# Kernel tuning notes

Hardware: AMD Instinct MI355X
Metric: run time of the kernel (lower is better)

The kernel has to match this reference:

```python
import jax, jax.numpy as jnp
import numpy as np

L, BS, H, W, C, NH = 6, 2, 48, 192, 128, 8
DIM = C // NH
EPS_LN = 1e-5
EPS_LA = 1e-6


def layer_norm(x, g, b):
    m = x.mean(-1, keepdims=True)
    v = ((x - m) ** 2).mean(-1, keepdims=True)
    return (x - m) / jnp.sqrt(v + EPS_LN) * g + b


def lin(x, w):
    # torch nn.Linear convention: y = x @ W^T
    return jnp.einsum('...i,oi->...o', x, w)


def linear_attention(q, k, v):
    # LoFTR-style kernelized attention: phi(x) = elu(x) + 1
    Q = jax.nn.elu(q) + 1.0
    K = jax.nn.elu(k) + 1.0
    KV = jnp.einsum('nshd,nshv->nhdv', K, v)            # [n, nh, d, d]
    Z = 1.0 / (jnp.einsum('nlhd,nhd->nlh', Q, K.sum(1)) + EPS_LA)
    return jnp.einsum('nlhd,nhdv,nlh->nlhv', Q, KV, Z)  # [n, l, nh, d]


def full_attention(q, k, v):
    scale = 1.0 / np.sqrt(q.shape[-1])
    qk = jnp.einsum('nlhd,nshd->nlsh', q, k) * scale    # [n, l, s, nh]
    A = jax.nn.softmax(qk, axis=2)
    out = jnp.einsum('nlsh,nshd->nlhd', A, v)
    return out, A


def self_layer(x, p):
    bs, h, w, c = x.shape
    xf = x.reshape(bs, h * w, c)
    xn = layer_norm(xf, p['n1_g'], p['n1_b'])
    q = lin(xn, p['q']).reshape(bs, h * w, NH, DIM)
    k = lin(xn, p['k']).reshape(bs, h * w, NH, DIM)
    v = lin(xn, p['v']).reshape(bs, h * w, NH, DIM)
    msg = linear_attention(q, k, v).reshape(bs, h * w, c)
    msg = xf + lin(msg, p['merge'])
    mn = layer_norm(msg, p['n2_g'], p['n2_b'])
    mn = lin(jax.nn.gelu(lin(mn, p['mlp1']), approximate=False), p['mlp2'])
    return (msg + mn).reshape(bs, h, w, c)


def cross_layer(fl, fr, p):
    bs, h, w, c = fl.shape
    fln = layer_norm(fl, p['n1_g'], p['n1_b'])
    frn = layer_norm(fr, p['n1_g'], p['n1_b'])

    def proj(x, wm):
        return lin(x, wm).reshape(bs * h, w, NH, DIM)

    ql, kl, vl = proj(fln, p['q']), proj(fln, p['k']), proj(fln, p['v'])
    qr, kr, vr = proj(frn, p['q']), proj(frn, p['k']), proj(frn, p['v'])

    def half(feat, q, k, v):
        msg, A = full_attention(q, k, v)
        raw = A.sum(-1).reshape(bs, h, w, w)
        m = feat + lin(msg.reshape(bs, h, w, c), p['merge'])
        mn = layer_norm(m, p['n2_g'], p['n2_b'])
        mn = lin(jax.nn.gelu(lin(mn, p['mlp1']), approximate=False), p['mlp2'])
        return m + mn, raw

    ml, raw_l = half(fl, ql, kr, vr)
    mr, raw_r = half(fr, qr, kl, vl)
    return ml, mr, raw_l, raw_r


PARAM_NAMES = ['q', 'k', 'v', 'merge', 'mlp1', 'mlp2']
VEC_NAMES = ['n1_g', 'n1_b', 'n2_g', 'n2_b']


def setup_inputs() -> dict:
    key = jax.random.key(0)
    ks = jax.random.split(key, 16)
    s = 1.0 / np.sqrt(C)
    inp = {
        'feat_left': jax.random.normal(ks[0], (BS, H, W, C), jnp.float32),
        'feat_right': jax.random.normal(ks[1], (BS, H, W, C), jnp.float32),
        'attn_left': jnp.zeros((BS, H, W, W), jnp.float32),
        'attn_right': jnp.zeros((BS, H, W, W), jnp.float32),
    }
    for i, nm in enumerate(PARAM_NAMES):
        inp['sa_' + nm] = jax.random.normal(ks[2 + i], (L, C, C), jnp.float32) * s
        inp['ca_' + nm] = jax.random.normal(ks[8 + i], (L, C, C), jnp.float32) * s
    for nm in VEC_NAMES:
        fill = jnp.ones if nm.endswith('_g') else jnp.zeros
        inp['sa_' + nm] = fill((L, C), jnp.float32)
        inp['ca_' + nm] = fill((L, C), jnp.float32)
    return inp


def reference(feat_left, feat_right, attn_left, attn_right,
              sa_q, sa_k, sa_v, sa_merge, sa_mlp1, sa_mlp2,
              sa_n1_g, sa_n1_b, sa_n2_g, sa_n2_b,
              ca_q, ca_k, ca_v, ca_merge, ca_mlp1, ca_mlp2,
              ca_n1_g, ca_n1_b, ca_n2_g, ca_n2_b):
    sa = {'q': sa_q, 'k': sa_k, 'v': sa_v, 'merge': sa_merge, 'mlp1': sa_mlp1,
          'mlp2': sa_mlp2, 'n1_g': sa_n1_g, 'n1_b': sa_n1_b, 'n2_g': sa_n2_g, 'n2_b': sa_n2_b}
    ca = {'q': ca_q, 'k': ca_k, 'v': ca_v, 'merge': ca_merge, 'mlp1': ca_mlp1,
          'mlp2': ca_mlp2, 'n1_g': ca_n1_g, 'n1_b': ca_n1_b, 'n2_g': ca_n2_g, 'n2_b': ca_n2_b}
    fl, fr, al, ar = feat_left, feat_right, attn_left, attn_right
    for i in range(L):
        p_sa = {k_: v_[i] for k_, v_ in sa.items()}
        p_ca = {k_: v_[i] for k_, v_ in ca.items()}
        fl = self_layer(fl, p_sa)
        fr = self_layer(fr, p_sa)
        fl, fr, raw_l, raw_r = cross_layer(fl, fr, p_ca)
        al = al + raw_l
        ar = ar + raw_r
    return fl, fr, (al, ar)
```

## Files before the change

kernel.cpp:

```cpp
#include <hip/hip_runtime.h>
#include <hip/hip_bf16.h>

using bf16x8 = __attribute__((ext_vector_type(8))) short;
using bf16x4 = __attribute__((ext_vector_type(4))) short;
using f32x4  = __attribute__((ext_vector_type(4))) float;

#define NE      4718592
#define HALF_R  18432
#define HALF_E  2359296
#define ATTN_E  3538944
#define SEQ     9216
#define NCHUNK  18
#define VSTRIDE 3088
#define RB_G    3136

typedef const unsigned int __attribute__((address_space(1)))* gas_u32;
typedef unsigned int __attribute__((address_space(3)))* las_u32;

__device__ __forceinline__ float b2f(short s) {
  union { unsigned u; float f; } x; x.u = ((unsigned)(unsigned short)s) << 16; return x.f;
}
__device__ __forceinline__ short f2b(float f) {
  __hip_bfloat16 h = __float2bfloat16(f);
  short s; __builtin_memcpy(&s, &h, 2); return s;
}
__device__ __forceinline__ f32x4 mfma16(bf16x8 a, bf16x8 b, f32x4 c) {
  return __builtin_amdgcn_mfma_f32_16x16x32_bf16(a, b, c, 0, 0, 0);
}
__device__ __forceinline__ f32x4 mfma16k16(bf16x4 a, bf16x4 b, f32x4 c) {
#if __has_builtin(__builtin_amdgcn_mfma_f32_16x16x16bf16_1k)
  return __builtin_amdgcn_mfma_f32_16x16x16bf16_1k(a, b, c, 0, 0, 0);
#else
  f32x4 d;
  asm("v_mfma_f32_16x16x16_bf16 %0, %1, %2, %3" : "=v"(d) : "v"(a), "v"(b), "v"(c));
  return d;
#endif
}

#define TR_READ12(V0,V1,V2,V3,V4,V5,V6,V7,V8,V9,V10,V11, ADDR) \
  asm volatile( \
    "ds_read_b64_tr_b16 %0, %12 offset:0\n\t" \
    "ds_read_b64_tr_b16 %1, %12 offset:512\n\t" \
    "ds_read_b64_tr_b16 %2, %12 offset:1024\n\t" \
    "ds_read_b64_tr_b16 %3, %12 offset:1536\n\t" \
    "ds_read_b64_tr_b16 %4, %12 offset:2048\n\t" \
    "ds_read_b64_tr_b16 %5, %12 offset:2560\n\t" \
    "ds_read_b64_tr_b16 %6, %12 offset:3072\n\t" \
    "ds_read_b64_tr_b16 %7, %12 offset:3584\n\t" \
    "ds_read_b64_tr_b16 %8, %12 offset:4096\n\t" \
    "ds_read_b64_tr_b16 %9, %12 offset:4608\n\t" \
    "ds_read_b64_tr_b16 %10, %12 offset:5120\n\t" \
    "ds_read_b64_tr_b16 %11, %12 offset:5632\n\t" \
    "s_waitcnt lgkmcnt(0)" \
    : "=&v"(V0), "=&v"(V1), "=&v"(V2), "=&v"(V3), "=&v"(V4), "=&v"(V5), \
      "=&v"(V6), "=&v"(V7), "=&v"(V8), "=&v"(V9), "=&v"(V10), "=&v"(V11) \
    : "v"(ADDR))

__global__ void k_w2b(const float* s0, const float* s1, const float* s2, const float* s3,
                      const float* s4, const float* s5, const float* s6, const float* s7,
                      const float* s8, const float* s9, const float* s10, const float* s11,
                      short* __restrict__ dst) {
  const float* srcs[12] = {s0,s1,s2,s3,s4,s5,s6,s7,s8,s9,s10,s11};
  const float* src = srcs[blockIdx.y];
  short* d = dst + (size_t)blockIdx.y*6*16384;
  int idx = blockIdx.x*256 + threadIdx.x;
  int layer = idx >> 11, w = idx & 2047;
  int c = w >> 4, gp = w & 15;
  int gs = gp ^ (c & 7);
  const float* s = src + layer*16384 + c*128 + gs*8;
  f32x4 v0 = *(const f32x4*)(s);
  f32x4 v1 = *(const f32x4*)(s + 4);
  short tmp[8];
  tmp[0]=f2b(v0[0]); tmp[1]=f2b(v0[1]); tmp[2]=f2b(v0[2]); tmp[3]=f2b(v0[3]);
  tmp[4]=f2b(v1[0]); tmp[5]=f2b(v1[1]); tmp[6]=f2b(v1[2]); tmp[7]=f2b(v1[3]);
  bf16x8 pk; __builtin_memcpy(&pk, tmp, 16);
  *(bf16x8*)(d + layer*16384 + c*128 + gp*8) = pk;
}

__device__ __forceinline__ void stage_W_async(const short* __restrict__ Wt, short* Ws,
                                              int wave, int lane) {
  #pragma unroll
  for (int is = 0; is < 8; is++) {
    int chunk = is*4 + wave;
    __builtin_amdgcn_global_load_lds((gas_u32)(const void*)(Wt + chunk*512 + lane*8),
                                     (las_u32)(void*)(Ws + chunk*512), 16, 0, 0);
  }
}
__device__ __forceinline__ void mfma_core_regA(const bf16x8 af[4], const short* Ws,
                                               int lane, f32x4 acc[8]) {
  int lrow = lane & 15, lgrp = lane >> 4;
  #pragma unroll
  for (int ct = 0; ct < 8; ct++) {
    int c = ct*16 + lrow;
    #pragma unroll
    for (int kc = 0; kc < 4; kc++) {
      int g = (kc*4 + lgrp) ^ (c & 7);
      bf16x8 wf = *(const bf16x8*)(&Ws[c*128 + g*8]);
      acc[ct] = mfma16(wf, af[kc], acc[ct]);
    }
  }
}
__device__ __forceinline__ void mfma_core_T(const short* As, const short* Ws,
                                            int wave, int lane, f32x4 acc[8]) {
  int lrow = lane & 15, lgrp = lane >> 4;
  bf16x8 af[4];
  int rl = wave*16 + lrow;
  #pragma unroll
  for (int kc = 0; kc < 4; kc++) {
    int g = (kc*4 + lgrp) ^ (rl & 7);
    af[kc] = *(const bf16x8*)(&As[rl*128 + g*8]);
  }
  mfma_core_regA(af, Ws, lane, acc);
}

__global__ __launch_bounds__(256) void k_qkv3(const float* __restrict__ FL,
                                              const float* __restrict__ FR,
                                              const short* __restrict__ Wq,
                                              const short* __restrict__ Wk,
                                              const short* __restrict__ Wv,
                                              const float* __restrict__ g,
                                              const float* __restrict__ b,
                                              short* __restrict__ Qo,
                                              short* __restrict__ Ko,
                                              short* __restrict__ Vo,
                                              int phi_mask, float qscale) {
  __shared__ short Ws[128*128];
  int tid = threadIdx.x;
  int row0 = blockIdx.x * 64;
  int wave = tid >> 6, lane = tid & 63;
  int lrow = lane & 15, lgrp = lane >> 4;
  int rl = wave*16 + lrow;
  int row = row0 + rl;
  const float* Fb = (row0 < HALF_R) ? FL : (FR - (size_t)HALF_E);
  stage_W_async(Wq, Ws, wave, lane);
  float x[4][8];
  const float* fr = Fb + (size_t)row*128;
  #pragma unroll
  for (int kc = 0; kc < 4; kc++) {
    f32x4 v0 = *(const f32x4*)(fr + kc*32 + lgrp*8);
    f32x4 v1 = *(const f32x4*)(fr + kc*32 + lgrp*8 + 4);
    x[kc][0]=v0[0]; x[kc][1]=v0[1]; x[kc][2]=v0[2]; x[kc][3]=v0[3];
    x[kc][4]=v1[0]; x[kc][5]=v1[1]; x[kc][6]=v1[2]; x[kc][7]=v1[3];
  }
  float s = 0.f, sq = 0.f;
  #pragma unroll
  for (int kc = 0; kc < 4; kc++)
    #pragma unroll
    for (int j = 0; j < 8; j++) { float xx = x[kc][j]; s += xx; sq += xx*xx; }
  s += __shfl_xor(s, 16, 64); sq += __shfl_xor(sq, 16, 64);
  s += __shfl_xor(s, 32, 64); sq += __shfl_xor(sq, 32, 64);
  float mean = s * (1.f/128.f);
  float var  = sq * (1.f/128.f) - mean*mean;
  float inv  = rsqrtf(var + 1e-5f);
  bf16x8 af[4];
  #pragma unroll
  for (int kc = 0; kc < 4; kc++) {
    int c0 = kc*32 + lgrp*8;
    f32x4 g0 = *(const f32x4*)(g + c0), g1 = *(const f32x4*)(g + c0 + 4);
    f32x4 b0 = *(const f32x4*)(b + c0), b1 = *(const f32x4*)(b + c0 + 4);
    short t8[8];
    t8[0]=f2b((x[kc][0]-mean)*inv*g0[0]+b0[0]); t8[1]=f2b((x[kc][1]-mean)*inv*g0[1]+b0[1]);
    t8[2]=f2b((x[kc][2]-mean)*inv*g0[2]+b0[2]); t8[3]=f2b((x[kc][3]-mean)*inv*g0[3]+b0[3]);
    t8[4]=f2b((x[kc][4]-mean)*inv*g1[0]+b1[0]); t8[5]=f2b((x[kc][5]-mean)*inv*g1[1]+b1[1]);
    t8[6]=f2b((x[kc][6]-mean)*inv*g1[2]+b1[2]); t8[7]=f2b((x[kc][7]-mean)*inv*g1[3]+b1[3]);
    __builtin_memcpy(&af[kc], t8, 16);
  }
  const short* Wp[3] = {Wq, Wk, Wv};
  short* Op[3] = {Qo, Ko, Vo};
  for (int y = 0; y < 3; y++) {
    __syncthreads();
    f32x4 acc[8] = {};
    mfma_core_regA(af, Ws, lane, acc);
    bool phi = (phi_mask >> y) & 1;
    float sc = (y == 0) ? qscale : 1.0f;
    short* OUT = Op[y] + (size_t)row*128 + lgrp*4;
    __syncthreads();
    if (y < 2) stage_W_async(Wp[y+1], Ws, wave, lane);
    #pragma unroll
    for (int ct = 0; ct < 8; ct++) {
      short t4[4];
      #pragma unroll
      for (int reg = 0; reg < 4; reg++) {
        float v = acc[ct][reg] * sc;
        if (phi) v = (v > 0.f) ? v + 1.0f : __expf(v);
        t4[reg] = f2b(v);
      }
      bf16x4 pk; __builtin_memcpy(&pk, t4, 8);
      *(bf16x4*)(OUT + ct*16) = pk;
    }
  }
}

template<bool REGA>
__device__ __forceinline__ void mlp_tail(const bf16x8 af1[4], short* As, short* Ws,
                                         const short* __restrict__ W1,
                                         const short* __restrict__ W2,
                                         const float* __restrict__ g,
                                         const float* __restrict__ b,
                                         const float* __restrict__ Fin,
                                         float* __restrict__ Fout,
                                         int row0, int tid) {
  int wave = tid >> 6, lane = tid & 63;
  int lrow = lane & 15, lgrp = lane >> 4;
  int rl = wave*16 + lrow;
  int orow = row0 + rl;
  const float* Fri = Fin + (size_t)orow*128 + lgrp*4;
  float* Fro = Fout + (size_t)orow*128 + lgrp*4;
  f32x4 acc[8] = {};
  if (REGA) mfma_core_regA(af1, Ws, lane, acc);
  else      mfma_core_T(As, Ws, wave, lane, acc);
  f32x4 fnew[8];
  #pragma unroll
  for (int ct = 0; ct < 8; ct++) {
    f32x4 fv = *(const f32x4*)(Fri + ct*16);
    fnew[ct] = acc[ct] + fv;
  }
  float s = 0.f, sq = 0.f;
  #pragma unroll
  for (int ct = 0; ct < 8; ct++)
    #pragma unroll
    for (int reg = 0; reg < 4; reg++) { float x = fnew[ct][reg]; s += x; sq += x*x; }
  s += __shfl_xor(s, 16, 64); sq += __shfl_xor(sq, 16, 64);
  s += __shfl_xor(s, 32, 64); sq += __shfl_xor(sq, 32, 64);
  float mean = s * (1.f/128.f);
  float var  = sq * (1.f/128.f) - mean*mean;
  float inv  = rsqrtf(var + 1e-5f);
  __syncthreads();
  stage_W_async(W1, Ws, wave, lane);
  #pragma unroll
  for (int ct = 0; ct < 8; ct++) {
    short t4[4];
    #pragma unroll
    for (int reg = 0; reg < 4; reg++) {
      int c = ct*16 + lgrp*4 + reg;
      t4[reg] = f2b((fnew[ct][reg] - mean) * inv * g[c] + b[c]);
    }
    bf16x4 pk; __builtin_memcpy(&pk, t4, 8);
    int G = ct*2 + (lgrp >> 1);
    *(bf16x4*)(&As[rl*128 + ((G ^ (rl & 7))*8) + (lgrp & 1)*4]) = pk;
  }
  __syncthreads();
  f32x4 acc2[8] = {};
  mfma_core_T(As, Ws, wave, lane, acc2);
  __syncthreads();
  stage_W_async(W2, Ws, wave, lane);
  #pragma unroll
  for (int ct = 0; ct < 8; ct++) {
    short t4[4];
    #pragma unroll
    for (int reg = 0; reg < 4; reg++) {
      float v = acc2[ct][reg];
      v = 0.5f*v*(1.0f + erff(v*0.70710678118654752f));
      t4[reg] = f2b(v);
    }
    bf16x4 pk; __builtin_memcpy(&pk, t4, 8);
    int G = ct*2 + (lgrp >> 1);
    *(bf16x4*)(&As[rl*128 + ((G ^ (rl & 7))*8) + (lgrp & 1)*4]) = pk;
  }
  __syncthreads();
  f32x4 acc3[8] = {};
  mfma_core_T(As, Ws, wave, lane, acc3);
  #pragma unroll
  for (int ct = 0; ct < 8; ct++) {
    f32x4 o = fnew[ct] + acc3[ct];
    *(f32x4*)(Fro + ct*16) = o;
  }
}

__global__ __launch_bounds__(256) void k_mlp(const short* __restrict__ Msg,
                                             const short* __restrict__ Wm,
                                             const short* __restrict__ W1,
                                             const short* __restrict__ W2,
                                             const float* __restrict__ g,
                                             const float* __restrict__ b,
                                             const float* __restrict__ Fin,
                                             float* __restrict__ Fout) {
  __shared__ short As[64*128];
  __shared__ short Ws[128*128];
  int tid = threadIdx.x;
  int row0 = blockIdx.x * 64;
  int wave = tid >> 6, lane = tid & 63;
  int lgrp = lane >> 4;
  int row = row0 + wave*16 + (lane & 15);
  stage_W_async(Wm, Ws, wave, lane);
  bf16x8 af1[4];
  const short* mr = Msg + (size_t)row*128;
  #pragma unroll
  for (int kc = 0; kc < 4; kc++)
    af1[kc] = *(const bf16x8*)(mr + kc*32 + lgrp*8);
  __syncthreads();
  mlp_tail<true>(af1, As, Ws, W1, W2, g, b, Fin, Fout, row0, tid);
}

__global__ __launch_bounds__(256) void k_mlp_self(const short* __restrict__ Q,
                                                  const float* __restrict__ kvp,
                                                  const short* __restrict__ Wm,
                                                  const short* __restrict__ W1,
                                                  const short* __restrict__ W2,
                                                  const float* __restrict__ g,
                                                  const float* __restrict__ b,
                                                  const float* __restrict__ FL,
                                                  const float* __restrict__ FR,
                                                  float* __restrict__ Fout) {
  __shared__ short As[64*128];
  __shared__ short Ws[128*128];
  __shared__ float kvs[8*273];
  int tid = threadIdx.x;
  int row0 = blockIdx.x * 64;
  int n = row0 / SEQ;
  const float* Fin = (row0 < HALF_R) ? FL : (FR - (size_t)HALF_E);
  stage_W_async(Wm, Ws, tid >> 6, tid & 63);
  for (int i = tid; i < 8*272; i += 256) {
    int h = i / 272, j = i % 272;
    const float* src = kvp + ((size_t)(n*8 + h)*NCHUNK)*272 + j;
    float s = 0.f;
    #pragma unroll
    for (int c2 = 0; c2 < NCHUNK; c2++) s += src[(size_t)c2*272];
    kvs[h*273 + j] = s;
  }
  __syncthreads();
  int r = tid >> 2, qq = tid & 3;
  const short* qr = Q + (size_t)(row0 + r)*128;
  #pragma unroll
  for (int hh = 0; hh < 2; hh++) {
    int h = qq*2 + hh;
    bf16x8 q0 = *(const bf16x8*)(qr + h*16);
    bf16x8 q1 = *(const bf16x8*)(qr + h*16 + 8);
    float q[16];
    #pragma unroll
    for (int j = 0; j < 8; j++) { q[j] = b2f(q0[j]); q[8+j] = b2f(q1[j]); }
    const float* kvh = kvs + h*273;
    float z = 1e-6f;
    #pragma unroll
    for (int d = 0; d < 16; d++) z += q[d] * kvh[256 + d];
    float invz = 1.f / z;
    short o16[16];
    #pragma unroll
    for (int d2 = 0; d2 < 16; d2++) {
      float o = 0.f;
      #pragma unroll
      for (int d = 0; d < 16; d++) o += q[d] * kvh[d*16 + d2];
      o16[d2] = f2b(o * invz);
    }
    bf16x8 lo, hi; __builtin_memcpy(&lo, o16, 16); __builtin_memcpy(&hi, o16+8, 16);
    *(bf16x8*)(&As[r*128 + (((2*h)   ^ (r & 7))*8)]) = lo;
    *(bf16x8*)(&As[r*128 + (((2*h+1) ^ (r & 7))*8)]) = hi;
  }
  __syncthreads();
  mlp_tail<false>(nullptr, As, Ws, W1, W2, g, b, Fin, Fout, row0, tid);
}

__global__ __launch_bounds__(256) void k_linred(const short* __restrict__ K,
                                                const short* __restrict__ V,
                                                float* __restrict__ kvp) {
  int nh = blockIdx.x;
  int n = nh >> 3, h = nh & 7;
  int chunk = blockIdx.y;
  int r0 = chunk * (SEQ / NCHUNK);
  __shared__ float ks[64][17], vs[64][17];
  int tid = threadIdx.x;
  int d1 = tid >> 4, d2 = tid & 15;
  int rr = tid >> 2, q = tid & 3;
  float kv = 0.f, ksum = 0.f;
  for (int r = r0; r < r0 + SEQ/NCHUNK; r += 64) {
    __syncthreads();
    bf16x4 kk = *(const bf16x4*)(K + (size_t)(n*SEQ + r + rr)*128 + h*16 + q*4);
    bf16x4 vv = *(const bf16x4*)(V + (size_t)(n*SEQ + r + rr)*128 + h*16 + q*4);
    #pragma unroll
    for (int j = 0; j < 4; j++) { ks[rr][q*4+j] = b2f(kk[j]); vs[rr][q*4+j] = b2f(vv[j]); }
    __syncthreads();
    #pragma unroll
    for (int j = 0; j < 64; j++) {
      float kvl = ks[j][d1];
      kv   += kvl * vs[j][d2];
      ksum += kvl;
    }
  }
  float* dst = kvp + ((size_t)nh*NCHUNK + chunk)*272;
  dst[d1*16 + d2] = kv;
  if (d2 == 0) dst[256 + d1] = ksum;
}

__global__ __launch_bounds__(512, 4) void k_fullattn(const short* __restrict__ Q,
                                                     const short* __restrict__ K,
                                                     const short* __restrict__ V,
                                                     short* __restrict__ MSG,
                                                     const float* __restrict__ RSL,
                                                     const float* __restrict__ RSR,
                                                     float* __restrict__ RDL,
                                                     float* __restrict__ RDR,
                                                     const float* __restrict__ ATL,
                                                     const float* __restrict__ ATR,
                                                     int first, int last) {
  __shared__ __attribute__((aligned(16))) char smem[4*RB_G*4];
  short* Vsub = (short*)smem;
  float* rawb = (float*)smem;
  int flat = blockIdx.x;
  int xcd = flat & 7, slot = flat >> 3;
  int group = xcd*24 + (slot >> 2);
  int part = slot & 3;
  int side = group >= 96 ? 1 : 0;
  int n = group - side*96;
  int qbase = side*HALF_R + n*192;
  int kbase = (side^1)*HALF_R + n*192;
  const float* rsb = (side ? RSR : RSL) + (size_t)n*192*192;
  float* rdb = (side ? RDR : RDL) + (size_t)n*192*192;
  const float* atb = (side ? ATR : ATL) + (size_t)n*192*192;
  int tid = threadIdx.x;
  int wave = tid >> 6, lane = tid & 63;
  int lrow = lane & 15, lgrp = lane >> 4;

  #pragma unroll
  for (int i = 0; i < 6; i++) {
    int c = tid + 512*i;
    int s = c >> 4, t8 = c & 15;
    bf16x8 v8 = *(const bf16x8*)(V + (size_t)(kbase + s)*128 + t8*8);
    *(bf16x8*)(&Vsub[(t8 >> 1)*VSTRIDE + s*16 + (t8 & 1)*8]) = v8;
  }
  __syncthreads();

  bf16x4 vf[12];
  {
    unsigned va = (unsigned)(uintptr_t)(&Vsub[0]) + wave*(VSTRIDE*2) + lane*8;
    TR_READ12(vf[0], vf[1], vf[2], vf[3], vf[4], vf[5],
              vf[6], vf[7], vf[8], vf[9], vf[10], vf[11], va);
  }
  __builtin_amdgcn_sched_barrier(0);
  bf16x4 kfr[12];
  #pragma unroll
  for (int st = 0; st < 12; st++)
    kfr[st] = *(const bf16x4*)(K + (size_t)(kbase + st*16 + lrow)*128
                                 + wave*16 + lgrp*4);
  __syncthreads();

  const f32x4 z4 = {0.f, 0.f, 0.f, 0.f};
  int g = wave & 3;
  for (int li = 0; li < 3; li++) {
    int l0 = (part*3 + li)*16;
    bf16x4 qf = *(const bf16x4*)(Q + (size_t)(qbase + l0 + lrow)*128 + wave*16 + lgrp*4);
    f32x4 sa[12];
    #pragma unroll
    for (int st = 0; st < 12; st++)
      sa[st] = mfma16k16(kfr[st], qf, z4);
    float m = -1e30f;
    #pragma unroll
    for (int st = 0; st < 12; st++)
      m = fmaxf(m, fmaxf(fmaxf(sa[st][0], sa[st][1]), fmaxf(sa[st][2], sa[st][3])));
    m = fmaxf(m, __shfl_xor(m, 16, 64));
    m = fmaxf(m, __shfl_xor(m, 32, 64));
    float sum = 0.f;
    #pragma unroll
    for (int st = 0; st < 12; st++) {
      #pragma unroll
      for (int r = 0; r < 4; r++) {
        float p = __expf(sa[st][r] - m);
        sa[st][r] = p; sum += p;
      }
    }
    sum += __shfl_xor(sum, 16, 64);
    sum += __shfl_xor(sum, 32, 64);
    float inv = 1.f / sum;
    #pragma unroll
    for (int st = 0; st < 12; st++) {
      sa[st][0] *= inv; sa[st][1] *= inv; sa[st][2] *= inv; sa[st][3] *= inv;
    }
    {
      f32x4 o = z4;
      #pragma unroll
      for (int st = 0; st < 12; st++) {
        bf16x4 pf;
        pf[0] = f2b(sa[st][0]); pf[1] = f2b(sa[st][1]);
        pf[2] = f2b(sa[st][2]); pf[3] = f2b(sa[st][3]);
        o = mfma16k16(vf[st], pf, o);
      }
      bf16x4 o4;
      o4[0] = f2b(o[0]); o4[1] = f2b(o[1]); o4[2] = f2b(o[2]); o4[3] = f2b(o[3]);
      *(bf16x4*)(MSG + (size_t)(qbase + l0 + lrow)*128 + wave*16 + lgrp*4) = o4;
    }
    if (wave < 4) {
      #pragma unroll
      for (int st = 0; st < 12; st++)
        *(f32x4*)(&rawb[g*RB_G + (lrow*49 + st*4 + lgrp)*4]) = sa[st];
    }
    __syncthreads();
    if (wave >= 4) {
      #pragma unroll
      for (int st = 0; st < 12; st++) {
        f32x4* slot2 = (f32x4*)(&rawb[g*RB_G + (lrow*49 + st*4 + lgrp)*4]);
        *slot2 = *slot2 + sa[st];
      }
    }
    __syncthreads();
    #pragma unroll
    for (int i = 0; i < 2; i++) {
      int sl = tid + 512*i;
      if (sl < 768) {
        int row = sl / 48, grp = sl - row*48;
        int off = (row*49 + grp)*4;
        f32x4 a = *(const f32x4*)(&rawb[0*RB_G + off]);
        f32x4 b = *(const f32x4*)(&rawb[1*RB_G + off]);
        f32x4 c = *(const f32x4*)(&rawb[2*RB_G + off]);
        f32x4 d = *(const f32x4*)(&rawb[3*RB_G + off]);
        f32x4 t = (a + b) + (c + d);
        size_t goff = (size_t)(l0 + row)*192 + grp*4;
        if (!first) t = t + *(const f32x4*)(rsb + goff);
        if (last)   t = t + *(const f32x4*)(atb + goff);
        *(f32x4*)(rdb + goff) = t;
      }
    }
    __syncthreads();
  }
}

extern "C" void kernel_launch(void* const* d_in, const int* in_sizes, int n_in,
                              void* d_out, int out_size, void* d_ws, size_t ws_size,
                              hipStream_t stream) {
  const float* feat_l = (const float*)d_in[0];
  const float* feat_r = (const float*)d_in[1];
  const float* attn_l = (const float*)d_in[2];
  const float* attn_r = (const float*)d_in[3];
  const float* saw[6] = { (const float*)d_in[4],  (const float*)d_in[6],  (const float*)d_in[8],
                          (const float*)d_in[10], (const float*)d_in[12], (const float*)d_in[14] };
  const float* caw[6] = { (const float*)d_in[5],  (const float*)d_in[7],  (const float*)d_in[9],
                          (const float*)d_in[11], (const float*)d_in[13], (const float*)d_in[15] };
  const float* sa_n1g = (const float*)d_in[16]; const float* ca_n1g = (const float*)d_in[17];
  const float* sa_n1b = (const float*)d_in[18]; const float* ca_n1b = (const float*)d_in[19];
  const float* sa_n2g = (const float*)d_in[20]; const float* ca_n2g = (const float*)d_in[21];
  const float* sa_n2b = (const float*)d_in[22]; const float* ca_n2b = (const float*)d_in[23];

  float* F   = (float*)d_ws;
  float* ALa = F + NE;
  float* ARa = ALa + ATTN_E;
  float* KVp = ARa + ATTN_E;
  short* WB  = (short*)(KVp + 32*NCHUNK*272);
  short* Qb  = WB + 12*6*16384;
  short* Kb  = Qb + NE;
  short* Vb  = Kb + NE;
  short* Mb  = Vb + NE;

  float* out = (float*)d_out;

  k_w2b<<<dim3(48,12), 256, 0, stream>>>(saw[0],saw[1],saw[2],saw[3],saw[4],saw[5],
                                         caw[0],caw[1],caw[2],caw[3],caw[4],caw[5], WB);

  for (int i = 0; i < 6; i++) {
    const short* sw[6], *cw[6];
    for (int t = 0; t < 6; t++) { sw[t] = WB + (size_t)(t*6 + i)*16384; cw[t] = WB + (size_t)((6+t)*6 + i)*16384; }
    int vo = i*128;
    const float* FL = (i == 0) ? feat_l : F;
    const float* FR = (i == 0) ? feat_r : (F + HALF_E);
    k_qkv3<<<576, 256, 0, stream>>>(FL, FR, sw[0], sw[1], sw[2], sa_n1g+vo, sa_n1b+vo,
                                    Qb, Kb, Vb, 0b011, 1.0f);
    k_linred<<<dim3(32, NCHUNK), 256, 0, stream>>>(Kb, Vb, KVp);
    k_mlp_self<<<576, 256, 0, stream>>>(Qb, KVp, sw[3], sw[4], sw[5],
                                        sa_n2g+vo, sa_n2b+vo, FL, FR, F);
    k_qkv3<<<576, 256, 0, stream>>>(F, F + HALF_E, cw[0], cw[1], cw[2],
                                    ca_n1g+vo, ca_n1b+vo, Qb, Kb, Vb, 0, 0.25f);
    int last = (i == 5);
    k_fullattn<<<768, 512, 0, stream>>>(Qb, Kb, Vb, Mb,
                                        ALa, ARa,
                                        last ? out + NE : ALa,
                                        last ? out + NE + ATTN_E : ARa,
                                        attn_l, attn_r,
                                        i == 0 ? 1 : 0, last);
    k_mlp<<<576, 256, 0, stream>>>(Mb, cw[3], cw[4], cw[5], ca_n2g+vo, ca_n2b+vo,
                                   F, last ? out : F);
  }
}
```

Baseline: 976.8 us.

## Fuse next-stage LayerNorm and QKV projection into MLP tail kernels

The separate QKV projection kernels run after each MLP are removed. The MLP tail kernels now keep their output rows in registers, apply the next stage's LayerNorm, and run the Q/K/V matmuls in the same block. The self-attention MLP produces cross-attention QKV, and the cross-attention MLP produces the next layer's self-attention QKV. This avoids launches and a full re-read of the fp32 feature buffer, at the cost of longer kernels with more register pressure and extra weight staging per block.

Measured after the change: 984.6 us. About the same (+0.8%).

```diff
diff --git a/kernel.cpp b/kernel.cpp
--- a/kernel.cpp
+++ b/kernel.cpp
@@ -191,7 +191,7 @@
   }
 }
 
-template<bool REGA>
+template<bool REGA, bool QKV>
 __device__ __forceinline__ void mlp_tail(const bf16x8 af1[4], short* As, short* Ws,
                                          const short* __restrict__ W1,
                                          const short* __restrict__ W2,
@@ -199,7 +199,16 @@
                                          const float* __restrict__ b,
                                          const float* __restrict__ Fin,
                                          float* __restrict__ Fout,
-                                         int row0, int tid) {
+                                         int row0, int tid,
+                                         const float* __restrict__ n1g,
+                                         const float* __restrict__ n1b,
+                                         const short* __restrict__ Wq,
+                                         const short* __restrict__ Wk,
+                                         const short* __restrict__ Wv,
+                                         short* __restrict__ Qo,
+                                         short* __restrict__ Ko,
+                                         short* __restrict__ Vo,
+                                         int phi_mask, float qscale) {
   int wave = tid >> 6, lane = tid & 63;
   int lrow = lane & 15, lgrp = lane >> 4;
   int rl = wave*16 + lrow;
@@ -260,10 +269,68 @@
   __syncthreads();
   f32x4 acc3[8] = {};
   mfma_core_T(As, Ws, wave, lane, acc3);
+  f32x4 o8[8];
   #pragma unroll
   for (int ct = 0; ct < 8; ct++) {
-    f32x4 o = fnew[ct] + acc3[ct];
-    *(f32x4*)(Fro + ct*16) = o;
+    o8[ct] = fnew[ct] + acc3[ct];
+    *(f32x4*)(Fro + ct*16) = o8[ct];
+  }
+  if (QKV) {
+    float s2 = 0.f, sq2 = 0.f;
+    #pragma unroll
+    for (int ct = 0; ct < 8; ct++)
+      #pragma unroll
+      for (int reg = 0; reg < 4; reg++) { float x = o8[ct][reg]; s2 += x; sq2 += x*x; }
+    s2 += __shfl_xor(s2, 16, 64); sq2 += __shfl_xor(sq2, 16, 64);
+    s2 += __shfl_xor(s2, 32, 64); sq2 += __shfl_xor(sq2, 32, 64);
+    float mean2 = s2 * (1.f/128.f);
+    float var2  = sq2 * (1.f/128.f) - mean2*mean2;
+    float inv2  = rsqrtf(var2 + 1e-5f);
+    __syncthreads();
+    stage_W_async(Wq, Ws, wave, lane);
+    #pragma unroll
+    for (int ct = 0; ct < 8; ct++) {
+      short t4[4];
+      #pragma unroll
+      for (int reg = 0; reg < 4; reg++) {
+        int c = ct*16 + lgrp*4 + reg;
+        t4[reg] = f2b((o8[ct][reg] - mean2) * inv2 * n1g[c] + n1b[c]);
+      }
+      bf16x4 pk; __builtin_memcpy(&pk, t4, 8);
+      int G = ct*2 + (lgrp >> 1);
+      *(bf16x4*)(&As[rl*128 + ((G ^ (rl & 7))*8) + (lgrp & 1)*4]) = pk;
+    }
+    __syncthreads();
+    bf16x8 af[4];
+    #pragma unroll
+    for (int kc = 0; kc < 4; kc++) {
+      int g2 = (kc*4 + lgrp) ^ (rl & 7);
+      af[kc] = *(const bf16x8*)(&As[rl*128 + g2*8]);
+    }
+    const short* Wp[3] = {Wq, Wk, Wv};
+    short* Op[3] = {Qo, Ko, Vo};
+    for (int y = 0; y < 3; y++) {
+      if (y > 0) __syncthreads();
+      f32x4 accq[8] = {};
+      mfma_core_regA(af, Ws, lane, accq);
+      __syncthreads();
+      if (y < 2) stage_W_async(Wp[y+1], Ws, wave, lane);
+      bool phi = (phi_mask >> y) & 1;
+      float sc = (y == 0) ? qscale : 1.0f;
+      short* OUT = Op[y] + (size_t)orow*128 + lgrp*4;
+      #pragma unroll
+      for (int ct = 0; ct < 8; ct++) {
+        short t4[4];
+        #pragma unroll
+        for (int reg = 0; reg < 4; reg++) {
+          float v = accq[ct][reg] * sc;
+          if (phi) v = (v > 0.f) ? v + 1.0f : __expf(v);
+          t4[reg] = f2b(v);
+        }
+        bf16x4 pk; __builtin_memcpy(&pk, t4, 8);
+        *(bf16x4*)(OUT + ct*16) = pk;
+      }
+    }
   }
 }
 
@@ -289,19 +356,63 @@
   for (int kc = 0; kc < 4; kc++)
     af1[kc] = *(const bf16x8*)(mr + kc*32 + lgrp*8);
   __syncthreads();
-  mlp_tail<true>(af1, As, Ws, W1, W2, g, b, Fin, Fout, row0, tid);
-}
-
-__global__ __launch_bounds__(256) void k_mlp_self(const short* __restrict__ Q,
-                                                  const float* __restrict__ kvp,
-                                                  const short* __restrict__ Wm,
-                                                  const short* __restrict__ W1,
-                                                  const short* __restrict__ W2,
-                                                  const float* __restrict__ g,
-                                                  const float* __restrict__ b,
-                                                  const float* __restrict__ FL,
-                                                  const float* __restrict__ FR,
-                                                  float* __restrict__ Fout) {
+  mlp_tail<true, false>(af1, As, Ws, W1, W2, g, b, Fin, Fout, row0, tid,
+                        nullptr, nullptr, nullptr, nullptr, nullptr,
+                        nullptr, nullptr, nullptr, 0, 0.f);
+}
+
+__global__ __launch_bounds__(256) void k_mlp_qkv(const short* __restrict__ Msg,
+                                                 const short* __restrict__ Wm,
+                                                 const short* __restrict__ W1,
+                                                 const short* __restrict__ W2,
+                                                 const float* __restrict__ g,
+                                                 const float* __restrict__ b,
+                                                 const float* __restrict__ Fin,
+                                                 float* __restrict__ Fout,
+                                                 const float* __restrict__ n1g,
+                                                 const float* __restrict__ n1b,
+                                                 const short* __restrict__ Wq,
+                                                 const short* __restrict__ Wk,
+                                                 const short* __restrict__ Wv,
+                                                 short* __restrict__ Qo,
+                                                 short* __restrict__ Ko,
+                                                 short* __restrict__ Vo) {
+  __shared__ short As[64*128];
+  __shared__ short Ws[128*128];
+  int tid = threadIdx.x;
+  int row0 = blockIdx.x * 64;
+  int wave = tid >> 6, lane = tid & 63;
+  int lgrp = lane >> 4;
+  int row = row0 + wave*16 + (lane & 15);
+  stage_W_async(Wm, Ws, wave, lane);
+  bf16x8 af1[4];
+  const short* mr = Msg + (size_t)row*128;
+  #pragma unroll
+  for (int kc = 0; kc < 4; kc++)
+    af1[kc] = *(const bf16x8*)(mr + kc*32 + lgrp*8);
+  __syncthreads();
+  mlp_tail<true, true>(af1, As, Ws, W1, W2, g, b, Fin, Fout, row0, tid,
+                       n1g, n1b, Wq, Wk, Wv, Qo, Ko, Vo, 0b011, 1.0f);
+}
+
+__global__ __launch_bounds__(256) void k_mlpself_qkv(const short* __restrict__ Q,
+                                                     const float* __restrict__ kvp,
+                                                     const short* __restrict__ Wm,
+                                                     const short* __restrict__ W1,
+                                                     const short* __restrict__ W2,
+                                                     const float* __restrict__ g,
+                                                     const float* __restrict__ b,
+                                                     const float* __restrict__ FL,
+                                                     const float* __restrict__ FR,
+                                                     float* __restrict__ Fout,
+                                                     const float* __restrict__ n1g,
+                                                     const float* __restrict__ n1b,
+                                                     const short* __restrict__ Wq,
+                                                     const short* __restrict__ Wk,
+                                                     const short* __restrict__ Wv,
+                                                     short* __restrict__ Qo,
+                                                     short* __restrict__ Ko,
+                                                     short* __restrict__ Vo) {
   __shared__ short As[64*128];
   __shared__ short Ws[128*128];
   __shared__ float kvs[8*273];
@@ -347,7 +458,8 @@
     *(bf16x8*)(&As[r*128 + (((2*h+1) ^ (r & 7))*8)]) = hi;
   }
   __syncthreads();
-  mlp_tail<false>(nullptr, As, Ws, W1, W2, g, b, Fin, Fout, row0, tid);
+  mlp_tail<false, true>(nullptr, As, Ws, W1, W2, g, b, Fin, Fout, row0, tid,
+                        n1g, n1b, Wq, Wk, Wv, Qo, Ko, Vo, 0, 0.25f);
 }
 
 __global__ __launch_bounds__(256) void k_linred(const short* __restrict__ K,
@@ -543,19 +655,25 @@
   k_w2b<<<dim3(48,12), 256, 0, stream>>>(saw[0],saw[1],saw[2],saw[3],saw[4],saw[5],
                                          caw[0],caw[1],caw[2],caw[3],caw[4],caw[5], WB);
 
+  {
+    const short* sw0[3] = { WB + (size_t)(0*6 + 0)*16384,
+                            WB + (size_t)(1*6 + 0)*16384,
+                            WB + (size_t)(2*6 + 0)*16384 };
+    k_qkv3<<<576, 256, 0, stream>>>(feat_l, feat_r, sw0[0], sw0[1], sw0[2],
+                                    sa_n1g, sa_n1b, Qb, Kb, Vb, 0b011, 1.0f);
+  }
+
   for (int i = 0; i < 6; i++) {
     const short* sw[6], *cw[6];
     for (int t = 0; t < 6; t++) { sw[t] = WB + (size_t)(t*6 + i)*16384; cw[t] = WB + (size_t)((6+t)*6 + i)*16384; }
     int vo = i*128;
     const float* FL = (i == 0) ? feat_l : F;
     const float* FR = (i == 0) ? feat_r : (F + HALF_E);
-    k_qkv3<<<576, 256, 0, stream>>>(FL, FR, sw[0], sw[1], sw[2], sa_n1g+vo, sa_n1b+vo,
-                                    Qb, Kb, Vb, 0b011, 1.0f);
     k_linred<<<dim3(32, NCHUNK), 256, 0, stream>>>(Kb, Vb, KVp);
-    k_mlp_self<<<576, 256, 0, stream>>>(Qb, KVp, sw[3], sw[4], sw[5],
-                                        sa_n2g+vo, sa_n2b+vo, FL, FR, F);
-    k_qkv3<<<576, 256, 0, stream>>>(F, F + HALF_E, cw[0], cw[1], cw[2],
-                                    ca_n1g+vo, ca_n1b+vo, Qb, Kb, Vb, 0, 0.25f);
+    k_mlpself_qkv<<<576, 256, 0, stream>>>(Qb, KVp, sw[3], sw[4], sw[5],
+                                           sa_n2g+vo, sa_n2b+vo, FL, FR, F,
+                                           ca_n1g+vo, ca_n1b+vo,
+                                           cw[0], cw[1], cw[2], Qb, Kb, Vb);
     int last = (i == 5);
     k_fullattn<<<768, 512, 0, stream>>>(Qb, Kb, Vb, Mb,
                                         ALa, ARa,
@@ -563,7 +681,17 @@
                                         last ? out + NE + ATTN_E : ARa,
                                         attn_l, attn_r,
                                         i == 0 ? 1 : 0, last);
-    k_mlp<<<576, 256, 0, stream>>>(Mb, cw[3], cw[4], cw[5], ca_n2g+vo, ca_n2b+vo,
-                                   F, last ? out : F);
-  }
-}
+    if (!last) {
+      const short* swn[3] = { WB + (size_t)(0*6 + i+1)*16384,
+                              WB + (size_t)(1*6 + i+1)*16384,
+                              WB + (size_t)(2*6 + i+1)*16384 };
+      k_mlp_qkv<<<576, 256, 0, stream>>>(Mb, cw[3], cw[4], cw[5],
+                                         ca_n2g+vo, ca_n2b+vo, F, F,
+                                         sa_n1g+(i+1)*128, sa_n1b+(i+1)*128,
+                                         swn[0], swn[1], swn[2], Qb, Kb, Vb);
+    } else {
+      k_mlp<<<576, 256, 0, stream>>>(Mb, cw[3], cw[4], cw[5],
+                                     ca_n2g+vo, ca_n2b+vo, F, out);
+    }
+  }
+}
```
